# Optimization experiments

Hardware: AMD Instinct MI355X
Metric: run time of the kernel (lower is better)

Reference implementation:

```python
import jax, jax.numpy as jnp
import numpy as np

DIM = 512
HEADS = 8
DIM_HEAD = 64
DIM_INNER = HEADS * DIM_HEAD
SCALE = DIM_HEAD ** -0.5


def setup_inputs() -> dict:
    key = jax.random.key(0)
    ks = jax.random.split(key, 8)
    b, n = 2, 1024
    x = jax.random.normal(ks[0], (b, n, DIM), dtype=jnp.float32)
    w = lambda k, i, o: jax.random.normal(k, (i, o), dtype=jnp.float32) * 0.02
    return {
        'x': x,
        'w_q_u': w(ks[1], DIM, DIM_INNER),
        'w_k_u': w(ks[2], DIM, DIM_INNER),
        'w_v_u': w(ks[3], DIM, DIM_INNER),
        'w_q_c': w(ks[4], DIM, DIM_INNER),
        'w_k_c': w(ks[5], DIM, DIM_INNER),
        'w_v_c': w(ks[6], DIM, DIM_INNER),
        'w_out': w(ks[7], DIM_INNER, DIM),
    }


def reference(x, w_q_u, w_k_u, w_v_u, w_q_c, w_k_c, w_v_c, w_out):
    b, n, _ = x.shape

    def proj(w):  # [b,n,dim] -> [b,h,n,d]
        return (x @ w).reshape(b, n, HEADS, DIM_HEAD).transpose(0, 2, 1, 3)

    q_u, k_u, v_u = proj(w_q_u), proj(w_k_u), proj(w_v_u)
    q_c, k_c, v_c = proj(w_q_c), proj(w_k_c), proj(w_v_c)

    idx = jnp.arange(n)
    causal = idx[:, None] >= idx[None, :]  # tril ones (binary causal mask)

    # term1 = (q_c @ v_u^T) * scale, zeroed above diagonal
    term1 = jnp.einsum('bhid,bhjd->bhij', q_c, v_u) * SCALE
    term1 = term1 * causal.astype(term1.dtype)

    # sigmoid term: (q_u @ k_u^T)*scale with lookahead mask tril(-inf, diag=0)
    logits_u = jnp.einsum('bhid,bhjd->bhij', q_u, k_u) * SCALE
    sig = jax.nn.sigmoid(jnp.where(causal, -jnp.inf, logits_u))

    # S_u[i,k] = sum_j term1[i,j] * sig[k,j]
    S_u = jnp.einsum('bhij,bhkj->bhik', term1, sig)

    # S_c: causal-masked QK
    S_c = jnp.einsum('bhid,bhjd->bhij', q_c, k_c) * SCALE
    S_c = jnp.where(causal, S_c, -jnp.inf)

    final_scores = S_c - jax.nn.silu(S_u)
    attn = jax.nn.softmax(final_scores, axis=-1)
    out = jnp.einsum('bhij,bhjd->bhid', attn, v_c)  # [b,h,n,d]
    out = out.transpose(0, 2, 1, 3).reshape(b, n, DIM_INNER)
    return out @ w_out
```

## Files before the change

### kernel.cpp

```cpp
#include <hip/hip_runtime.h>
#include <math.h>


typedef __bf16 bf16x8 __attribute__((ext_vector_type(8)));
typedef float f32x4 __attribute__((ext_vector_type(4)));

#define SCALE 0.125f

#define GLL(g, l) __builtin_amdgcn_global_load_lds(                         \
    (const __attribute__((address_space(1))) void*)(g),                     \
    (__attribute__((address_space(3))) void*)(l), 16, 0, 0)

__device__ __forceinline__ unsigned short f2bf(float f){
  unsigned int x = __builtin_bit_cast(unsigned int, f);
  unsigned int r = (x + 0x7fffu + ((x >> 16) & 1u)) >> 16;
  return (unsigned short)r;
}
__device__ __forceinline__ float bf2f(unsigned short u){
  unsigned int x = ((unsigned int)u) << 16;
  return __builtin_bit_cast(float, x);
}
__device__ __forceinline__ f32x4 mfma16(bf16x8 a, bf16x8 b, f32x4 c){
  return __builtin_amdgcn_mfma_f32_16x16x32_bf16(a, b, c, 0, 0, 0);
}
__device__ __forceinline__ bf16x8 ld8(const unsigned short* p){
  return *(const bf16x8*)p;
}

__device__ const unsigned char QK_CUM[16] =
  {0,1,2,4,6,9,12,16,20,25,30,36,42,49,56,64};

__device__ const unsigned char SC_RB[72] =
  {15,14,11,13,15,10,12,14,15,14,13,12,15,13,11, 9,
   12, 8, 6,15,13,11, 9, 7,15,13,14,10,14,12,10, 8,
    9, 3,14,12,10, 8, 6, 4,15,13,11, 7,11, 9, 7, 5,
   13,10, 8,11, 9, 6, 4, 2,15,14,12, 5, 7, 5, 3, 1,
   14,12,10, 8, 6, 4, 2, 0};
__device__ const unsigned char SC_CT[72] =
  { 1, 1, 0, 1, 2, 0, 1, 2, 0, 0, 0, 0, 3, 2, 1, 0,
    3, 1, 0, 4, 3, 2, 1, 0, 5, 4, 4, 2, 3, 2, 1, 0,
    3, 0, 5, 4, 3, 2, 1, 0, 6, 5, 4, 2, 3, 2, 1, 0,
    6, 4, 3, 5, 4, 2, 1, 0, 7, 6, 5, 1, 3, 2, 1, 0,
    7, 6, 5, 4, 3, 2, 1, 0};

__global__ __launch_bounds__(256) void k_prep(
    const float* __restrict__ x,
    const float* __restrict__ w0, const float* __restrict__ w1,
    const float* __restrict__ w2, const float* __restrict__ w3,
    const float* __restrict__ w4, const float* __restrict__ w5,
    const float* __restrict__ w6,
    unsigned short* __restrict__ xb, unsigned short* __restrict__ wT){
  int t = threadIdx.x;
  if (blockIdx.x < 576){
    for (int i = blockIdx.x * 256 + t; i < 262144; i += 576 * 256){
      float4 v = ((const float4*)x)[i];
      ushort4 o; o.x = f2bf(v.x); o.y = f2bf(v.y); o.z = f2bf(v.z); o.w = f2bf(v.w);
      ((ushort4*)xb)[i] = o;
    }
    return;
  }
  __shared__ float lds[64 * 65];
  int bx = blockIdx.x - 576;
  int mat = bx >> 6, tile = bx & 63, tr = tile >> 3, tc = tile & 7;
  int k0 = tr * 64, c0 = tc * 64;
  const float* src;
  switch (mat){
    case 0: src = w0; break; case 1: src = w1; break; case 2: src = w2; break;
    case 3: src = w3; break; case 4: src = w4; break; case 5: src = w5; break;
    default: src = w6; break;
  }
#pragma unroll
  for (int i = 0; i < 4; ++i){
    int r = (t >> 4) + i * 16, c4 = (t & 15) * 4;
    float4 v = *(const float4*)(src + (size_t)(k0 + r) * 512 + c0 + c4);
    lds[r * 65 + c4 + 0] = v.x; lds[r * 65 + c4 + 1] = v.y;
    lds[r * 65 + c4 + 2] = v.z; lds[r * 65 + c4 + 3] = v.w;
  }
  __syncthreads();
  unsigned short* dst = wT + (size_t)mat * 262144;
#pragma unroll
  for (int i = 0; i < 4; ++i){
    int oc = (t >> 4) + i * 16;
    int kq = (t & 15) * 4;
    ushort4 o;
    o.x = f2bf(lds[(kq + 0) * 65 + oc]);
    o.y = f2bf(lds[(kq + 1) * 65 + oc]);
    o.z = f2bf(lds[(kq + 2) * 65 + oc]);
    o.w = f2bf(lds[(kq + 3) * 65 + oc]);
    *(ushort4*)(dst + (size_t)(c0 + oc) * 512 + k0 + kq) = o;
  }
}

__global__ __launch_bounds__(256) void k_proj(
    const unsigned short* __restrict__ xb, const unsigned short* __restrict__ wT,
    unsigned short* __restrict__ P){
  __shared__ unsigned short sA[2 * 64 * 32], sB[2 * 128 * 32];
  int t = threadIdx.x, lane = t & 63, l16 = lane & 15, quad = lane >> 4;
  int w = t >> 6, wm = w >> 1, wn = w & 1;
  int bx = blockIdx.x;
  int mt = bx / 24, nt = bx - mt * 24;
  int M0 = mt * 64, N0 = nt * 128;
  int matb = N0 >> 9;
  int nin = N0 & 511;
  int srow = (lane >> 2), scol = (lane & 3) * 8;
  const unsigned short* gA = xb + (size_t)(M0 + w*16 + srow) * 512 + scol;
  const unsigned short* gB = wT + (size_t)matb * 262144
                               + (size_t)(nin + w*32 + srow) * 512 + scol;
  unsigned short* lA0 = sA + (w*16) * 32;
  unsigned short* lB0 = sB + (w*32) * 32;
  unsigned short* lA1 = lA0 + 64 * 32;
  unsigned short* lB1 = lB0 + 128 * 32;
  f32x4 acc[4][2] = {};
  for (int k0 = 0; k0 < 512; k0 += 64){
    GLL(gA + k0,               lA0);
    GLL(gB + k0,               lB0);
    GLL(gB + k0 + 16*512,      lB0 + 16*32);
    GLL(gA + k0 + 32,          lA1);
    GLL(gB + k0 + 32,          lB1);
    GLL(gB + k0 + 32 + 16*512, lB1 + 16*32);
    __syncthreads();
#pragma unroll
    for (int h = 0; h < 2; ++h){
      bf16x8 aw[4], ax[2];
#pragma unroll
      for (int fi = 0; fi < 4; ++fi)
        aw[fi] = *(const bf16x8*)(sB + h*4096 + (wn*64 + fi*16 + l16) * 32 + quad * 8);
#pragma unroll
      for (int mi = 0; mi < 2; ++mi)
        ax[mi] = *(const bf16x8*)(sA + h*2048 + (wm*32 + mi*16 + l16) * 32 + quad * 8);
#pragma unroll
      for (int fi = 0; fi < 4; ++fi)
#pragma unroll
        for (int mi = 0; mi < 2; ++mi)
          acc[fi][mi] = mfma16(aw[fi], ax[mi], acc[fi][mi]);
    }
    __syncthreads();
  }
#pragma unroll
  for (int fi = 0; fi < 4; ++fi)
#pragma unroll
    for (int mi = 0; mi < 2; ++mi){
      int row = M0 + wm*32 + mi*16 + l16;
      int b_ = row >> 10, n_ = row & 1023;
      int c0 = N0 + wn*64 + fi*16 + quad*4;
      int h = (c0 & 511) >> 6, d = c0 & 63;
      int bh = b_*8 + h;
      ushort4 o;
      o.x = f2bf(acc[fi][mi][0]); o.y = f2bf(acc[fi][mi][1]);
      o.z = f2bf(acc[fi][mi][2]); o.w = f2bf(acc[fi][mi][3]);
      *(ushort4*)(P + (size_t)(matb*16 + bh) * 65536 + (size_t)n_ * 64 + d) = o;
    }
}

__global__ __launch_bounds__(256) void k_qk_vct(
    const unsigned short* __restrict__ P,
    unsigned short* __restrict__ term1, unsigned short* __restrict__ sig,
    unsigned short* __restrict__ vcT){
  int t = threadIdx.x;
  if (blockIdx.x < 256){
    __shared__ unsigned short lds[64 * 72];
    int bh = blockIdx.x >> 4, nt = blockIdx.x & 15;
    int N0 = nt * 64;
    const unsigned short* src = P + (size_t)(5*16 + bh) * 65536 + (size_t)N0 * 64;
#pragma unroll
    for (int i2 = 0; i2 < 2; ++i2){
      int id = i2 * 256 + t;
      int r = id >> 3, c8 = (id & 7) * 8;
      ushort4 v0 = *(const ushort4*)(src + r * 64 + c8);
      ushort4 v1 = *(const ushort4*)(src + r * 64 + c8 + 4);
      *(ushort4*)(lds + r * 72 + c8) = v0;
      *(ushort4*)(lds + r * 72 + c8 + 4) = v1;
    }
    __syncthreads();
    unsigned short* dst = vcT + (size_t)bh * 65536;
#pragma unroll
    for (int i2 = 0; i2 < 2; ++i2){
      int id = i2 * 256 + t;
      int dd = id >> 3, n8 = (id & 7) * 8;
      ushort4 a, b;
      a.x = lds[(n8+0)*72 + dd]; a.y = lds[(n8+1)*72 + dd];
      a.z = lds[(n8+2)*72 + dd]; a.w = lds[(n8+3)*72 + dd];
      b.x = lds[(n8+4)*72 + dd]; b.y = lds[(n8+5)*72 + dd];
      b.z = lds[(n8+6)*72 + dd]; b.w = lds[(n8+7)*72 + dd];
      *(ushort4*)(dst + (size_t)dd * 1024 + N0 + n8) = a;
      *(ushort4*)(dst + (size_t)dd * 1024 + N0 + n8 + 4) = b;
    }
    return;
  }
  __shared__ unsigned short sA[2 * 64 * 32], sB[2 * 128 * 32];
  int id = blockIdx.x - 256;
  int bh = id & 15, tt = id >> 4;
  int mat = (tt >= 72);
  int tl = mat ? tt - 72 : tt;
  int rb = 15;
  while (QK_CUM[rb] > tl) --rb;
  int ct = tl - QK_CUM[rb];
  int R0, C0;
  const unsigned short *Asrc, *Bsrc;
  if (!mat){ R0 = rb * 64;        C0 = ct * 128;
             Asrc = P + (size_t)(3*16 + bh) * 65536;
             Bsrc = P + (size_t)(2*16 + bh) * 65536; }
  else     { R0 = (15 - rb) * 64; C0 = (7 - ct) * 128;
             Asrc = P + (size_t)(0*16 + bh) * 65536;
             Bsrc = P + (size_t)(1*16 + bh) * 65536; }
  int lane = t & 63, l16 = lane & 15, quad = lane >> 4;
  int w = t >> 6, wm = w >> 1, wn = w & 1;
  int srow = lane >> 2, scol = (lane & 3) * 8;
  const unsigned short* gA = Asrc + (size_t)(R0 + w*16 + srow) * 64 + scol;
  const unsigned short* gB = Bsrc + (size_t)(C0 + w*32 + srow) * 64 + scol;
  unsigned short* lA0 = sA + (w*16) * 32;
  unsigned short* lB0 = sB + (w*32) * 32;
  unsigned short* lA1 = lA0 + 64 * 32;
  unsigned short* lB1 = lB0 + 128 * 32;
  f32x4 acc[4][2] = {};
  GLL(gA,              lA0);
  GLL(gB,              lB0);
  GLL(gB + 16*64,      lB0 + 16*32);
  GLL(gA + 32,         lA1);
  GLL(gB + 32,         lB1);
  GLL(gB + 32 + 16*64, lB1 + 16*32);
  __syncthreads();
#pragma unroll
  for (int h = 0; h < 2; ++h){
    bf16x8 af[2], bfr[4];
#pragma unroll
    for (int mi = 0; mi < 2; ++mi)
      af[mi] = *(const bf16x8*)(sA + h*2048 + (wm*32 + mi*16 + l16) * 32 + quad * 8);
#pragma unroll
    for (int fi = 0; fi < 4; ++fi)
      bfr[fi] = *(const bf16x8*)(sB + h*4096 + (wn*64 + fi*16 + l16) * 32 + quad * 8);
#pragma unroll
    for (int fi = 0; fi < 4; ++fi)
#pragma unroll
      for (int mi = 0; mi < 2; ++mi)
        acc[fi][mi] = mfma16(bfr[fi], af[mi], acc[fi][mi]);
  }
  unsigned short* out = (mat ? sig : term1) + (size_t)bh * 1048576;
#pragma unroll
  for (int fi = 0; fi < 4; ++fi)
#pragma unroll
    for (int mi = 0; mi < 2; ++mi){
      int row = R0 + wm*32 + mi*16 + l16;
      int c0 = C0 + wn*64 + fi*16 + quad*4;
      ushort4 o;
#pragma unroll
      for (int r = 0; r < 4; ++r){
        int col = c0 + r;
        float v = acc[fi][mi][r] * SCALE;
        unsigned short res;
        if (!mat) res = (col <= row) ? f2bf(v) : (unsigned short)0;
        else      res = (col >  row) ? f2bf(1.f / (1.f + expf(-v))) : (unsigned short)0;
        ((unsigned short*)&o)[r] = res;
      }
      *(ushort4*)(out + (size_t)row * 1024 + c0) = o;
    }
}

__global__ __launch_bounds__(256) void k_scores(
    const unsigned short* __restrict__ P, const unsigned short* __restrict__ term1,
    const unsigned short* __restrict__ sig, unsigned short* __restrict__ finb){
  __shared__ unsigned short sA[2 * 64 * 32], sB[2 * 128 * 32];
  int t = threadIdx.x;
  int bh = blockIdx.x & 15, tt = blockIdx.x >> 4;
  int rb = SC_RB[tt], ct = SC_CT[tt];
  int R0 = rb * 64, C0 = ct * 128;
  size_t sbase = (size_t)bh * 1048576;
  int lane = t & 63, l16 = lane & 15, quad = lane >> 4;
  int w = t >> 6, wm = w >> 1, wn = w & 1;
  int srow = lane >> 2, scol = (lane & 3) * 8;
  unsigned short* lA0 = sA + (w*16) * 32;
  unsigned short* lB0 = sB + (w*32) * 32;
  unsigned short* lA1 = lA0 + 64 * 32;
  unsigned short* lB1 = lB0 + 128 * 32;
  f32x4 acc_u[4][2] = {};
  f32x4 acc_c[4][2] = {};
  {
    const unsigned short* gA = term1 + sbase + (size_t)(R0 + w*16 + srow) * 1024 + scol;
    const unsigned short* gB = sig   + sbase + (size_t)(C0 + w*32 + srow) * 1024 + scol;
    int nsteps = (R0 + 64 - C0) >> 5;
    for (int s = 0; s < nsteps; s += 2){
      int j0 = C0 + s * 32;
      int two = (s + 1 < nsteps);
      GLL(gA + j0,             lA0);
      GLL(gB + j0,             lB0);
      GLL(gB + j0 + 16*1024,   lB0 + 16*32);
      if (two){
        GLL(gA + j0 + 32,           lA1);
        GLL(gB + j0 + 32,           lB1);
        GLL(gB + j0 + 32 + 16*1024, lB1 + 16*32);
      }
      __syncthreads();
      for (int h = 0; h <= two; ++h){
        bf16x8 af[2], bfr[4];
#pragma unroll
        for (int mi = 0; mi < 2; ++mi)
          af[mi] = *(const bf16x8*)(sA + h*2048 + (wm*32 + mi*16 + l16) * 32 + quad * 8);
#pragma unroll
        for (int fi = 0; fi < 4; ++fi)
          bfr[fi] = *(const bf16x8*)(sB + h*4096 + (wn*64 + fi*16 + l16) * 32 + quad * 8);
#pragma unroll
        for (int fi = 0; fi < 4; ++fi)
#pragma unroll
          for (int mi = 0; mi < 2; ++mi)
            acc_u[fi][mi] = mfma16(bfr[fi], af[mi], acc_u[fi][mi]);
      }
      __syncthreads();
    }
  }
  {
    const unsigned short* Qc = P + (size_t)(3*16 + bh) * 65536;
    const unsigned short* Kc = P + (size_t)(4*16 + bh) * 65536;
#pragma unroll
    for (int k0 = 0; k0 < 64; k0 += 32){
      bf16x8 af[2], bfr[4];
#pragma unroll
      for (int mi = 0; mi < 2; ++mi)
        af[mi] = ld8(Qc + (size_t)(R0 + wm*32 + mi*16 + l16) * 64 + k0 + quad * 8);
#pragma unroll
      for (int fi = 0; fi < 4; ++fi)
        bfr[fi] = ld8(Kc + (size_t)(C0 + wn*64 + fi*16 + l16) * 64 + k0 + quad * 8);
#pragma unroll
      for (int fi = 0; fi < 4; ++fi)
#pragma unroll
        for (int mi = 0; mi < 2; ++mi)
          acc_c[fi][mi] = mfma16(bfr[fi], af[mi], acc_c[fi][mi]);
    }
  }
  unsigned short* out = finb + sbase;
#pragma unroll
  for (int fi = 0; fi < 4; ++fi)
#pragma unroll
    for (int mi = 0; mi < 2; ++mi){
      int row = R0 + wm*32 + mi*16 + l16;
      int c0 = C0 + wn*64 + fi*16 + quad*4;
      ushort4 o;
#pragma unroll
      for (int r = 0; r < 4; ++r){
        float su = acc_u[fi][mi][r];
        float v = acc_c[fi][mi][r] * SCALE - su / (1.f + expf(-su));
        ((unsigned short*)&o)[r] = f2bf(v);
      }
      *(ushort4*)(out + (size_t)row * 1024 + c0) = o;
    }
}

__global__ __launch_bounds__(256) void k_pv_soft(
    const unsigned short* __restrict__ finb, const unsigned short* __restrict__ vcT,
    unsigned short* __restrict__ O2){
  __shared__ __align__(16) unsigned char smem[16 * 1032 * 2];
  unsigned short* lp = (unsigned short*)smem;
  float* red = (float*)smem;
  int t = threadIdx.x;
  int bh = blockIdx.x & 15;
  int r4 = blockIdx.x >> 8, g = (blockIdx.x >> 4) & 15;
  int mt = (r4 == 0) ? 63 - g : (r4 == 1) ? 32 + g : (r4 == 2) ? 31 - g : g;
  int m0 = mt * 16;
  int kceil = ((m0 + 16 + 31) >> 5) << 5;
  {
    int rl = t >> 4, sub = t & 15;
    int rloc = m0 + rl;
    const unsigned short* p = finb + (size_t)bh * 1048576 + (size_t)rloc * 1024;
    float v[8][8];
    float m = -INFINITY;
#pragma unroll
    for (int i = 0; i < 8; ++i){
      int c8 = (sub + 16*i) * 8;
      if (c8 < kceil){
        ushort4 u0 = *(const ushort4*)(p + c8);
        ushort4 u1 = *(const ushort4*)(p + c8 + 4);
        float vv[8] = {bf2f(u0.x), bf2f(u0.y), bf2f(u0.z), bf2f(u0.w),
                       bf2f(u1.x), bf2f(u1.y), bf2f(u1.z), bf2f(u1.w)};
#pragma unroll
        for (int e = 0; e < 8; ++e){
          v[i][e] = (c8 + e <= rloc) ? vv[e] : -INFINITY;
          m = fmaxf(m, v[i][e]);
        }
      }
    }
#pragma unroll
    for (int off = 1; off < 16; off <<= 1) m = fmaxf(m, __shfl_xor(m, off));
    float s = 0.f;
#pragma unroll
    for (int i = 0; i < 8; ++i){
      int c8 = (sub + 16*i) * 8;
      if (c8 < kceil){
#pragma unroll
        for (int e = 0; e < 8; ++e){
          v[i][e] = expf(v[i][e] - m);
          s += v[i][e];
        }
      }
    }
#pragma unroll
    for (int off = 1; off < 16; off <<= 1) s += __shfl_xor(s, off);
    float inv = 1.f / s;
#pragma unroll
    for (int i = 0; i < 8; ++i){
      int c8 = (sub + 16*i) * 8;
      if (c8 < kceil){
        ushort4 o0, o1;
        o0.x = f2bf(v[i][0] * inv); o0.y = f2bf(v[i][1] * inv);
        o0.z = f2bf(v[i][2] * inv); o0.w = f2bf(v[i][3] * inv);
        o1.x = f2bf(v[i][4] * inv); o1.y = f2bf(v[i][5] * inv);
        o1.z = f2bf(v[i][6] * inv); o1.w = f2bf(v[i][7] * inv);
        *(ushort4*)(lp + rl * 1032 + c8) = o0;
        *(ushort4*)(lp + rl * 1032 + c8 + 4) = o1;
      }
    }
  }
  __syncthreads();
  int lane = t & 63, l16 = lane & 15, quad = lane >> 4, w = t >> 6;
  const unsigned short* Bt = vcT + (size_t)bh * 65536;
  int ktot = kceil >> 5;
  int per = (ktot + 3) >> 2;
  int s0 = w * per, s1 = min(s0 + per, ktot);
  f32x4 acc[4] = {};
  for (int s = s0; s < s1; ++s){
    int k0 = s * 32;
    bf16x8 a = *(const bf16x8*)(lp + l16 * 1032 + k0 + quad * 8);
#pragma unroll
    for (int fi = 0; fi < 4; ++fi){
      bf16x8 b = ld8(Bt + (size_t)(fi*16 + l16) * 1024 + k0 + quad * 8);
      acc[fi] = mfma16(a, b, acc[fi]);
    }
  }
  __syncthreads();
#pragma unroll
  for (int fi = 0; fi < 4; ++fi)
#pragma unroll
    for (int r = 0; r < 4; ++r)
      red[w * 1024 + (quad*4 + r) * 64 + fi*16 + l16] = acc[fi][r];
  __syncthreads();
  float4 a0 = ((const float4*)(red + 0*1024))[t];
  float4 a1 = ((const float4*)(red + 1*1024))[t];
  float4 a2 = ((const float4*)(red + 2*1024))[t];
  float4 a3 = ((const float4*)(red + 3*1024))[t];
  ushort4 o;
  o.x = f2bf(a0.x + a1.x + a2.x + a3.x);
  o.y = f2bf(a0.y + a1.y + a2.y + a3.y);
  o.z = f2bf(a0.z + a1.z + a2.z + a3.z);
  o.w = f2bf(a0.w + a1.w + a2.w + a3.w);
  int e = t * 4, row = e >> 6, col = e & 63;
  int b_ = bh >> 3, h_ = bh & 7;
  *(ushort4*)(O2 + (size_t)(b_*1024 + m0 + row) * 512 + h_*64 + col) = o;
}

__global__ __launch_bounds__(256) void k_out(
    const unsigned short* __restrict__ O2, const unsigned short* __restrict__ woT,
    float* __restrict__ out){
  __shared__ float red[4][1024];
  int t = threadIdx.x, lane = t & 63, l16 = lane & 15, quad = lane >> 4, w = t >> 6;
  int mt = blockIdx.x >> 3, nt = blockIdx.x & 7;
  int m0 = mt * 16, n0 = nt * 64;
  int r_ = m0 + l16;
  f32x4 acc[4] = {};
#pragma unroll
  for (int s = 0; s < 4; ++s){
    int kk = w * 128 + s * 32 + quad * 8;
    bf16x8 a = ld8(O2 + (size_t)r_ * 512 + kk);
#pragma unroll
    for (int fi = 0; fi < 4; ++fi){
      bf16x8 b = ld8(woT + (size_t)(n0 + fi*16 + l16) * 512 + kk);
      acc[fi] = mfma16(a, b, acc[fi]);
    }
  }
#pragma unroll
  for (int fi = 0; fi < 4; ++fi)
#pragma unroll
    for (int r = 0; r < 4; ++r)
      red[w][(quad*4 + r) * 64 + fi*16 + l16] = acc[fi][r];
  __syncthreads();
  float4 a0 = ((const float4*)red[0])[t];
  float4 a1 = ((const float4*)red[1])[t];
  float4 a2 = ((const float4*)red[2])[t];
  float4 a3 = ((const float4*)red[3])[t];
  float4 o;
  o.x = a0.x + a1.x + a2.x + a3.x;
  o.y = a0.y + a1.y + a2.y + a3.y;
  o.z = a0.z + a1.z + a2.z + a3.z;
  o.w = a0.w + a1.w + a2.w + a3.w;
  int e = t * 4, row = e >> 6, col = e & 63;
  *(float4*)(out + (size_t)(m0 + row) * 512 + n0 + col) = o;
}

extern "C" void kernel_launch(void* const* d_in, const int* in_sizes, int n_in,
                              void* d_out, int out_size, void* d_ws, size_t ws_size,
                              hipStream_t stream){
  const float* x = (const float*)d_in[0];
  float* out = (float*)d_out;
  unsigned short* ws = (unsigned short*)d_ws;

  unsigned short* wT    = ws;
  unsigned short* xb    = wT    + (size_t)7  * 262144;
  unsigned short* P     = xb    + (size_t)1048576;
  unsigned short* vcT   = P     + (size_t)96 * 65536;
  unsigned short* term1 = vcT   + (size_t)16 * 65536;
  unsigned short* sig   = term1 + (size_t)16 * 1048576;
  unsigned short* O2    = sig   + (size_t)16 * 1048576;
  unsigned short* finb  = O2    + (size_t)16 * 65536;

  k_prep<<<1024, 256, 0, stream>>>(
      x,
      (const float*)d_in[1], (const float*)d_in[2], (const float*)d_in[3],
      (const float*)d_in[4], (const float*)d_in[5], (const float*)d_in[6],
      (const float*)d_in[7], xb, wT);
  k_proj<<<768, 256, 0, stream>>>(xb, wT, P);
  k_qk_vct<<<2560, 256, 0, stream>>>(P, term1, sig, vcT);
  k_scores<<<1152, 256, 0, stream>>>(P, term1, sig, finb);
  k_pv_soft<<<1024, 256, 0, stream>>>(finb, vcT, O2);
  k_out<<<1024, 256, 0, stream>>>(O2, wT + (size_t)6 * 262144, out);
}
```

Measured before the change: 161.6 us.

## Double-buffer LDS tiles with async prefetch in projection and scores GEMMs

```diff
diff --git a/kernel.cpp b/kernel.cpp
--- a/kernel.cpp
+++ b/kernel.cpp
@@ -94,7 +94,8 @@
 __global__ __launch_bounds__(256) void k_proj(
     const unsigned short* __restrict__ xb, const unsigned short* __restrict__ wT,
     unsigned short* __restrict__ P){
-  __shared__ unsigned short sA[2 * 64 * 32], sB[2 * 128 * 32];
+  __shared__ __align__(16) unsigned short sA[2 * 2 * 64 * 32];
+  __shared__ __align__(16) unsigned short sB[2 * 2 * 128 * 32];
   int t = threadIdx.x, lane = t & 63, l16 = lane & 15, quad = lane >> 4;
   int w = t >> 6, wm = w >> 1, wn = w & 1;
   int bx = blockIdx.x;
@@ -106,36 +107,45 @@
   const unsigned short* gA = xb + (size_t)(M0 + w*16 + srow) * 512 + scol;
   const unsigned short* gB = wT + (size_t)matb * 262144
                                + (size_t)(nin + w*32 + srow) * 512 + scol;
-  unsigned short* lA0 = sA + (w*16) * 32;
-  unsigned short* lB0 = sB + (w*32) * 32;
-  unsigned short* lA1 = lA0 + 64 * 32;
-  unsigned short* lB1 = lB0 + 128 * 32;
+  unsigned short* lA = sA + (w*16) * 32;
+  unsigned short* lB = sB + (w*32) * 32;
   f32x4 acc[4][2] = {};
-  for (int k0 = 0; k0 < 512; k0 += 64){
-    GLL(gA + k0,               lA0);
-    GLL(gB + k0,               lB0);
-    GLL(gB + k0 + 16*512,      lB0 + 16*32);
-    GLL(gA + k0 + 32,          lA1);
-    GLL(gB + k0 + 32,          lB1);
-    GLL(gB + k0 + 32 + 16*512, lB1 + 16*32);
-    __syncthreads();
+#define STAGE_PROJ(buf, k0) do {                                   \
+    GLL(gA + (k0),               lA + (buf)*4096);                 \
+    GLL(gB + (k0),               lB + (buf)*8192);                 \
+    GLL(gB + (k0) + 16*512,      lB + (buf)*8192 + 16*32);         \
+    GLL(gA + (k0) + 32,          lA + (buf)*4096 + 2048);          \
+    GLL(gB + (k0) + 32,          lB + (buf)*8192 + 4096);          \
+    GLL(gB + (k0) + 32 + 16*512, lB + (buf)*8192 + 4096 + 16*32);  \
+  } while(0)
+  STAGE_PROJ(0, 0);
+  for (int it = 0; it < 8; ++it){
+    if (it < 7){
+      STAGE_PROJ((it+1) & 1, (it+1)*64);
+      asm volatile("s_waitcnt vmcnt(6)" ::: "memory");
+    } else {
+      asm volatile("s_waitcnt vmcnt(0)" ::: "memory");
+    }
+    __builtin_amdgcn_s_barrier();
+    int b = it & 1;
 #pragma unroll
     for (int h = 0; h < 2; ++h){
       bf16x8 aw[4], ax[2];
 #pragma unroll
       for (int fi = 0; fi < 4; ++fi)
-        aw[fi] = *(const bf16x8*)(sB + h*4096 + (wn*64 + fi*16 + l16) * 32 + quad * 8);
+        aw[fi] = *(const bf16x8*)(sB + b*8192 + h*4096 + (wn*64 + fi*16 + l16) * 32 + quad * 8);
 #pragma unroll
       for (int mi = 0; mi < 2; ++mi)
-        ax[mi] = *(const bf16x8*)(sA + h*2048 + (wm*32 + mi*16 + l16) * 32 + quad * 8);
+        ax[mi] = *(const bf16x8*)(sA + b*4096 + h*2048 + (wm*32 + mi*16 + l16) * 32 + quad * 8);
 #pragma unroll
       for (int fi = 0; fi < 4; ++fi)
 #pragma unroll
         for (int mi = 0; mi < 2; ++mi)
           acc[fi][mi] = mfma16(aw[fi], ax[mi], acc[fi][mi]);
     }
-    __syncthreads();
-  }
+    __builtin_amdgcn_s_barrier();
+  }
+#undef STAGE_PROJ
 #pragma unroll
   for (int fi = 0; fi < 4; ++fi)
 #pragma unroll
@@ -259,7 +269,8 @@
 __global__ __launch_bounds__(256) void k_scores(
     const unsigned short* __restrict__ P, const unsigned short* __restrict__ term1,
     const unsigned short* __restrict__ sig, unsigned short* __restrict__ finb){
-  __shared__ unsigned short sA[2 * 64 * 32], sB[2 * 128 * 32];
+  __shared__ __align__(16) unsigned short sA[2 * 2 * 64 * 32];
+  __shared__ __align__(16) unsigned short sB[2 * 2 * 128 * 32];
   int t = threadIdx.x;
   int bh = blockIdx.x & 15, tt = blockIdx.x >> 4;
   int rb = SC_RB[tt], ct = SC_CT[tt];
@@ -268,45 +279,22 @@
   int lane = t & 63, l16 = lane & 15, quad = lane >> 4;
   int w = t >> 6, wm = w >> 1, wn = w & 1;
   int srow = lane >> 2, scol = (lane & 3) * 8;
-  unsigned short* lA0 = sA + (w*16) * 32;
-  unsigned short* lB0 = sB + (w*32) * 32;
-  unsigned short* lA1 = lA0 + 64 * 32;
-  unsigned short* lB1 = lB0 + 128 * 32;
+  unsigned short* lA = sA + (w*16) * 32;
+  unsigned short* lB = sB + (w*32) * 32;
   f32x4 acc_u[4][2] = {};
   f32x4 acc_c[4][2] = {};
-  {
-    const unsigned short* gA = term1 + sbase + (size_t)(R0 + w*16 + srow) * 1024 + scol;
-    const unsigned short* gB = sig   + sbase + (size_t)(C0 + w*32 + srow) * 1024 + scol;
-    int nsteps = (R0 + 64 - C0) >> 5;
-    for (int s = 0; s < nsteps; s += 2){
-      int j0 = C0 + s * 32;
-      int two = (s + 1 < nsteps);
-      GLL(gA + j0,             lA0);
-      GLL(gB + j0,             lB0);
-      GLL(gB + j0 + 16*1024,   lB0 + 16*32);
-      if (two){
-        GLL(gA + j0 + 32,           lA1);
-        GLL(gB + j0 + 32,           lB1);
-        GLL(gB + j0 + 32 + 16*1024, lB1 + 16*32);
-      }
-      __syncthreads();
-      for (int h = 0; h <= two; ++h){
-        bf16x8 af[2], bfr[4];
-#pragma unroll
-        for (int mi = 0; mi < 2; ++mi)
-          af[mi] = *(const bf16x8*)(sA + h*2048 + (wm*32 + mi*16 + l16) * 32 + quad * 8);
-#pragma unroll
-        for (int fi = 0; fi < 4; ++fi)
-          bfr[fi] = *(const bf16x8*)(sB + h*4096 + (wn*64 + fi*16 + l16) * 32 + quad * 8);
-#pragma unroll
-        for (int fi = 0; fi < 4; ++fi)
-#pragma unroll
-          for (int mi = 0; mi < 2; ++mi)
-            acc_u[fi][mi] = mfma16(bfr[fi], af[mi], acc_u[fi][mi]);
-      }
-      __syncthreads();
-    }
-  }
+  const unsigned short* gA = term1 + sbase + (size_t)(R0 + w*16 + srow) * 1024 + scol;
+  const unsigned short* gB = sig   + sbase + (size_t)(C0 + w*32 + srow) * 1024 + scol;
+  int n_it = (R0 + 64 - C0) >> 6;
+#define STAGE_SC(buf, j0) do {                                      \
+    GLL(gA + (j0),                lA + (buf)*4096);                 \
+    GLL(gB + (j0),                lB + (buf)*8192);                 \
+    GLL(gB + (j0) + 16*1024,      lB + (buf)*8192 + 16*32);         \
+    GLL(gA + (j0) + 32,           lA + (buf)*4096 + 2048);          \
+    GLL(gB + (j0) + 32,           lB + (buf)*8192 + 4096);          \
+    GLL(gB + (j0) + 32 + 16*1024, lB + (buf)*8192 + 4096 + 16*32);  \
+  } while(0)
+  STAGE_SC(0, C0);
   {
     const unsigned short* Qc = P + (size_t)(3*16 + bh) * 65536;
     const unsigned short* Kc = P + (size_t)(4*16 + bh) * 65536;
@@ -326,6 +314,33 @@
           acc_c[fi][mi] = mfma16(bfr[fi], af[mi], acc_c[fi][mi]);
     }
   }
+  for (int it = 0; it < n_it; ++it){
+    if (it + 1 < n_it){
+      STAGE_SC((it+1) & 1, C0 + (it+1)*64);
+      asm volatile("s_waitcnt vmcnt(6)" ::: "memory");
+    } else {
+      asm volatile("s_waitcnt vmcnt(0)" ::: "memory");
+    }
+    __builtin_amdgcn_s_barrier();
+    int b = it & 1;
+#pragma unroll
+    for (int h = 0; h < 2; ++h){
+      bf16x8 af[2], bfr[4];
+#pragma unroll
+      for (int mi = 0; mi < 2; ++mi)
+        af[mi] = *(const bf16x8*)(sA + b*4096 + h*2048 + (wm*32 + mi*16 + l16) * 32 + quad * 8);
+#pragma unroll
+      for (int fi = 0; fi < 4; ++fi)
+        bfr[fi] = *(const bf16x8*)(sB + b*8192 + h*4096 + (wn*64 + fi*16 + l16) * 32 + quad * 8);
+#pragma unroll
+      for (int fi = 0; fi < 4; ++fi)
+#pragma unroll
+        for (int mi = 0; mi < 2; ++mi)
+          acc_u[fi][mi] = mfma16(bfr[fi], af[mi], acc_u[fi][mi]);
+    }
+    __builtin_amdgcn_s_barrier();
+  }
+#undef STAGE_SC
   unsigned short* out = finb + sbase;
 #pragma unroll
   for (int fi = 0; fi < 4; ++fi)
```

Result: no change. 161.4 us (-0.1%).
